# Kernel optimization log

Measured on AMD Instinct MI355X. Metric: run time of the kernel, lower is better.

## Reference

```python
import jax, jax.numpy as jnp
import numpy as np
from jax import lax

B, FREQ, TIME = 32, 256, 4096   # batch, freq bins, time frames
PAD_LEN = 256                   # cfg['n_peaks']
KSIZE = 5                       # cfg['blur_kernel']
SIGMA = 1.0                     # cfg['blur_sigma']


def setup_inputs() -> dict:
    key = jax.random.key(0)
    return {"spec_tensor": jax.random.normal(key, (B, FREQ, TIME), dtype=jnp.float32)}


def _peak_from_features(f):
    # local maxima along time (1x3) and freq (3x1), SAME padding, stride 1
    neg = jnp.asarray(-jnp.inf, f.dtype)
    max_t = lax.reduce_window(f, neg, lax.max, (1, 1, 3), (1, 1, 1), 'SAME')
    max_f = lax.reduce_window(f, neg, lax.max, (1, 3, 1), (1, 1, 1), 'SAME')
    peaks = ((f == max_t) & (f == max_f)).astype(f.dtype)
    mn = jnp.min(f, axis=(1, 2), keepdims=True)
    mx = jnp.max(f, axis=(1, 2), keepdims=True)
    return peaks * ((f - mn) / (mx - mn))


def _gaussian_blur(x):
    # separable gaussian blur with reflect padding (torchvision semantics)
    half = KSIZE // 2
    coords = jnp.arange(KSIZE, dtype=x.dtype) - half
    g = jnp.exp(-0.5 * (coords / SIGMA) ** 2)
    g = g / jnp.sum(g)
    x4 = jnp.pad(x, ((0, 0), (half, half), (half, half)), mode='reflect')[:, None]  # [B,1,F+2h,T+2h]
    kf = g.reshape(1, 1, KSIZE, 1)
    kt = g.reshape(1, 1, 1, KSIZE)
    y = lax.conv_general_dilated(x4, kf, (1, 1), 'VALID')
    y = lax.conv_general_dilated(y, kt, (1, 1), 'VALID')
    return y[:, 0]


def _extract(flat):
    # compact nonzero entries (row-major order) into fixed PAD_LEN slots, zero padded;
    # entries beyond PAD_LEN are truncated (scatter mode='drop').
    mask = flat > 0
    pos = jnp.cumsum(mask.astype(jnp.int32)) - 1
    dest = jnp.where(mask, pos, PAD_LEN)  # out-of-range -> dropped
    idx = jnp.zeros(PAD_LEN, jnp.int32).at[dest].set(
        jnp.arange(flat.shape[0], dtype=jnp.int32), mode='drop')
    val = jnp.zeros(PAD_LEN, flat.dtype).at[dest].set(flat, mode='drop')
    freq = (idx // TIME).astype(flat.dtype) / FREQ
    time = (idx % TIME).astype(flat.dtype) / TIME
    return jnp.stack([freq, time, val], axis=0)  # [3, PAD_LEN]


def reference(spec_tensor):
    p = _peak_from_features(spec_tensor)
    p = _gaussian_blur(p)
    p = _peak_from_features(p)
    return jax.vmap(_extract)(p.reshape(B, FREQ * TIME))  # [B, 3, PAD_LEN]
```

## Files before the change

kernel.cpp:

```cpp
#include <hip/hip_runtime.h>

#define NB 32
#define NF 256
#define NT 4096
#define PAD_LEN 256

#define TF 16
#define TT 128

#define TS 32
#define NSTRIP (NT / TS)

#define G0 0.054488684f
#define G1 0.24420134f
#define G2 0.40261995f

__device__ __forceinline__ float blur5(float a, float b, float c, float d, float e) {
    return G0 * (a + b) + G1 * (c + d) + G2 * e;
}
__device__ __forceinline__ float4 blur5v(const float4& a, const float4& b, const float4& c,
                                         const float4& d, const float4& e) {
    return make_float4(blur5(a.x, b.x, c.x, d.x, e.x), blur5(a.y, b.y, c.y, d.y, e.y),
                       blur5(a.z, b.z, c.z, d.z, e.z), blur5(a.w, b.w, c.w, d.w, e.w));
}

#define SW 140
#define SW4 35
#define RS 24
#define RP 22
#define RV 18

#define R1_WORDS (RS * SW)
#define R2_WORDS (RP * SW)

#define MPAD 12

__device__ __forceinline__ int reflectF(int i) {
    i = (i < 0) ? -i : i;
    return (i >= NF) ? (2 * NF - 2 - i) : i;
}
__device__ __forceinline__ unsigned encf(float x) {
    unsigned u = __float_as_uint(x);
    return (u & 0x80000000u) ? ~u : (u | 0x80000000u);
}
__device__ __forceinline__ float decf(unsigned e) {
    unsigned u = (e & 0x80000000u) ? (e ^ 0x80000000u) : ~e;
    return __uint_as_float(u);
}

#define MM_OFF 0
#define CNT_OFF 1024
#define PFX_OFF (1024 + NB * NF * 32 * 4)

__global__ __launch_bounds__(256) void k_init(float* __restrict__ out, unsigned* __restrict__ mm,
                                              int* __restrict__ counts2) {
    int tid = blockIdx.x * 256 + threadIdx.x;
    if (tid < NB * 3 * PAD_LEN) out[tid] = 0.0f;
    if (tid < NB) {
        mm[tid * 4 + 0] = 0xFFFFFFFFu;
        mm[tid * 4 + 1] = 0u;
        mm[tid * 4 + 2] = 0xFFFFFFFFu;
        mm[tid * 4 + 3] = 0u;
    }
    for (int i = tid; i < NB * NF * 32; i += 96 * 256) counts2[i] = 0;
}

__global__ __launch_bounds__(256) void k_minmax(const float* __restrict__ spec, unsigned* __restrict__ mm) {
    const int b = blockIdx.y;
    const float4* p = (const float4*)(spec + (size_t)b * NF * NT);
    const int base4 = blockIdx.x * 4096;
    float lmin = __builtin_inff(), lmax = -__builtin_inff();
    for (int i = threadIdx.x; i < 4096; i += 256) {
        float4 v = p[base4 + i];
        lmin = fminf(lmin, fminf(fminf(v.x, v.y), fminf(v.z, v.w)));
        lmax = fmaxf(lmax, fmaxf(fmaxf(v.x, v.y), fmaxf(v.z, v.w)));
    }
    for (int off = 32; off; off >>= 1) {
        lmin = fminf(lmin, __shfl_down(lmin, off));
        lmax = fmaxf(lmax, __shfl_down(lmax, off));
    }
    __shared__ float rmn[4], rmx[4];
    int wave = threadIdx.x >> 6, lane = threadIdx.x & 63;
    if (lane == 0) { rmn[wave] = lmin; rmx[wave] = lmax; }
    __syncthreads();
    if (threadIdx.x == 0) {
        for (int w = 1; w < 4; w++) { lmin = fminf(lmin, rmn[w]); lmax = fmaxf(lmax, rmx[w]); }
        atomicMin(&mm[b * 4 + 0], encf(lmin));
        atomicMax(&mm[b * 4 + 1], encf(lmax));
    }
}


template<int J> __device__ __forceinline__ float getj(const float4& v) {
    if constexpr (J == 0) return v.x;
    else if constexpr (J == 1) return v.y;
    else if constexpr (J == 2) return v.z;
    else return v.w;
}

template<bool DP, bool DH, bool DQ, int J>
__device__ __forceinline__ void march_step(
    const float4& r0, const float4& r1, const float4& r2, const float4& r3,
    float4& Sa, float4& Sb, float4& Sc,
    float4& V0, float4& V1, float4& V2, float4& V3, float4& V4,
    float4& Bm, float4& Bc, float4& Bp,
    int& c0, int& c1, int& c2, int& c3,
    float& lmin, float& lmax,
    const int lane, const int sid, const float mn, const float rinv, const int hb)
{
    const float NEGF = -__builtin_inff();
    float4 X = make_float4(getj<J>(r0), getj<J>(r1), getj<J>(r2), getj<J>(r3));
    Sa = Sb; Sb = Sc; Sc = X;
    if constexpr (DP) {
        float up0 = __shfl_up(Sb.w, 1);
        float dn3 = __shfl_down(Sb.x, 1);
        if (lane == 0)  up0 = NEGF;
        if (lane == 63) dn3 = NEGF;
        float4 P;
        { const float x = Sb.x; const bool pk = (x >= Sa.x) && (x >= Sc.x) && (x >= up0)  && (x >= Sb.y); P.x = pk ? (x - mn) * rinv : 0.0f; }
        { const float x = Sb.y; const bool pk = (x >= Sa.y) && (x >= Sc.y) && (x >= Sb.x) && (x >= Sb.z); P.y = pk ? (x - mn) * rinv : 0.0f; }
        { const float x = Sb.z; const bool pk = (x >= Sa.z) && (x >= Sc.z) && (x >= Sb.y) && (x >= Sb.w); P.z = pk ? (x - mn) * rinv : 0.0f; }
        { const float x = Sb.w; const bool pk = (x >= Sa.w) && (x >= Sc.w) && (x >= Sb.z) && (x >= dn3); P.w = pk ? (x - mn) * rinv : 0.0f; }
        const float pzm = __shfl_up(P.z, 1);
        const float pwm = __shfl_up(P.w, 1);
        const float pxp = __shfl_down(P.x, 1);
        const float pyp = __shfl_down(P.y, 1);
        float4 Vn;
        Vn.x = blur5(pzm, P.z, pwm, P.y, P.x);
        Vn.y = blur5(pwm, P.w, P.x, P.z, P.y);
        Vn.z = blur5(P.x, pxp, P.y, P.w, P.z);
        Vn.w = blur5(P.y, pyp, P.z, pxp, P.w);
        if (lane == 0)  { Vn.x = blur5(P.z, P.z, P.y, P.y, P.x);
                          Vn.y = blur5(P.y, P.w, P.x, P.z, P.y); }
        if (lane == 63) { Vn.z = blur5(P.x, P.z, P.y, P.w, P.z);
                          Vn.w = blur5(P.y, P.y, P.z, P.z, P.w); }
        V0 = V1; V1 = V2; V2 = V3; V3 = V4; V4 = Vn;
    }
    if constexpr (DH) {
        const int h = hb + J;
        float4 Bn;
        if ((unsigned)h < (unsigned)NT) {
            Bn = blur5v(V0, V4, V1, V3, V2);
            if (sid == 0) {
                if (h == 0)      Bn = blur5v(V4, V4, V3, V3, V2);
                else if (h == 1) Bn = blur5v(V2, V4, V1, V3, V2);
            }
            if (sid == NSTRIP - 1) {
                if (h == NT - 2)      Bn = blur5v(V0, V2, V1, V3, V2);
                else if (h == NT - 1) Bn = blur5v(V0, V0, V1, V1, V2);
            }
        } else {
            Bn = make_float4(NEGF, NEGF, NEGF, NEGF);
        }
        Bm = Bc; Bc = Bp; Bp = Bn;
    }
    if constexpr (DQ) {
        float u0 = __shfl_up(Bc.w, 1);
        float d3 = __shfl_down(Bc.x, 1);
        if (lane == 0)  u0 = NEGF;
        if (lane == 63) d3 = NEGF;
        { const float x = Bc.x; const bool pk = (x >= Bm.x) && (x >= Bp.x) && (x >= u0)   && (x >= Bc.y); c0 += (pk && (x > 0.0f)) ? 1 : 0; }
        { const float x = Bc.y; const bool pk = (x >= Bm.y) && (x >= Bp.y) && (x >= Bc.x) && (x >= Bc.z); c1 += (pk && (x > 0.0f)) ? 1 : 0; }
        { const float x = Bc.z; const bool pk = (x >= Bm.z) && (x >= Bp.z) && (x >= Bc.y) && (x >= Bc.w); c2 += (pk && (x > 0.0f)) ? 1 : 0; }
        { const float x = Bc.w; const bool pk = (x >= Bm.w) && (x >= Bp.w) && (x >= Bc.z) && (x >= d3); c3 += (pk && (x > 0.0f)) ? 1 : 0; }
        lmin = fminf(lmin, fminf(fminf(Bc.x, Bc.y), fminf(Bc.z, Bc.w)));
        lmax = fmaxf(lmax, fmaxf(fmaxf(Bc.x, Bc.y), fmaxf(Bc.z, Bc.w)));
    }
}

__global__ __launch_bounds__(256) void k_march(const float* __restrict__ spec,
                                               unsigned* __restrict__ mm,
                                               int* __restrict__ counts2) {
    const int b = blockIdx.y;
    const int lane = threadIdx.x & 63;
    const int wv = threadIdx.x >> 6;
    const int sid = blockIdx.x * 4 + wv;
    const int T0 = sid * TS;

    const float mn = decf(mm[b * 4 + 0]);
    const float mx = decf(mm[b * 4 + 1]);
    const float rinv = 1.0f / (mx - mn);

    const float NEGF = -__builtin_inff();
    const float4 NEG4 = make_float4(NEGF, NEGF, NEGF, NEGF);

    __shared__ __align__(16) float sStage[4][256 * MPAD];
    float* myS = sStage[wv];

    const int srow = lane >> 1;
    const int shalf = lane & 1;
    const float* gsrc = spec + (size_t)b * NF * NT + (size_t)srow * NT + 4 * shalf;

    float4 R[8];
    float4 A[4];

#define GLOAD(G) do {                                                          \
    const int tg = T0 - 4 + 8 * (G);                                           \
    const bool ok = (unsigned)(tg + 4 * shalf) < (unsigned)NT;                 \
    _Pragma("unroll")                                                          \
    for (int i = 0; i < 8; ++i)                                                \
        R[i] = ok ? *(const float4*)(gsrc + (size_t)(32 * i) * NT + tg) : NEG4; \
} while (0)

#define SWRITE() do {                                                          \
    _Pragma("unroll")                                                          \
    for (int i = 0; i < 8; ++i)                                                \
        *(float4*)(myS + (32 * i + srow) * MPAD + 4 * shalf) = R[i];           \
} while (0)

#define SREAD(c) do {                                                          \
    _Pragma("unroll")                                                          \
    for (int j = 0; j < 4; ++j)                                                \
        A[j] = *(const float4*)(myS + (4 * lane + j) * MPAD + (c));            \
} while (0)

    float4 Sa = NEG4, Sb = NEG4, Sc = NEG4;
    float4 V0 = NEG4, V1 = NEG4, V2 = NEG4, V3 = NEG4, V4 = NEG4;
    float4 Bm = NEG4, Bc = NEG4, Bp = NEG4;
    int c0 = 0, c1 = 0, c2 = 0, c3 = 0;
    float lmin = __builtin_inff(), lmax = NEGF;

#define MARGS Sa, Sb, Sc, V0, V1, V2, V3, V4, Bm, Bc, Bp, c0, c1, c2, c3, lmin, lmax, lane, sid, mn, rinv

    GLOAD(0);
    SWRITE();
    GLOAD(1);
    SREAD(0);
    march_step<false, false, false, 0>(A[0], A[1], A[2], A[3], MARGS, 0);
    march_step<false, false, false, 1>(A[0], A[1], A[2], A[3], MARGS, 0);
    march_step<true,  false, false, 2>(A[0], A[1], A[2], A[3], MARGS, 0);
    march_step<true,  false, false, 3>(A[0], A[1], A[2], A[3], MARGS, 0);
    SREAD(4);
    {
        const int hb = T0 - 3;
        march_step<true, false, false, 0>(A[0], A[1], A[2], A[3], MARGS, hb);
        march_step<true, false, false, 1>(A[0], A[1], A[2], A[3], MARGS, hb);
        march_step<true, true,  false, 2>(A[0], A[1], A[2], A[3], MARGS, hb);
        march_step<true, true,  false, 3>(A[0], A[1], A[2], A[3], MARGS, hb);
    }

#define STEADY_GROUP(G) do {                                                   \
    SWRITE();                                                                  \
    if ((G) < 4) GLOAD((G) + 1);                                               \
    SREAD(0);                                                                  \
    {                                                                          \
        const int hb = T0 + 8 * (G) - 7;           \
        march_step<true, true, true, 0>(A[0], A[1], A[2], A[3], MARGS, hb);    \
        march_step<true, true, true, 1>(A[0], A[1], A[2], A[3], MARGS, hb);    \
        march_step<true, true, true, 2>(A[0], A[1], A[2], A[3], MARGS, hb);    \
        march_step<true, true, true, 3>(A[0], A[1], A[2], A[3], MARGS, hb);    \
    }                                                                          \
    SREAD(4);                                                                  \
    {                                                                          \
        const int hb = T0 + 8 * (G) - 3;                         \
        march_step<true, true, true, 0>(A[0], A[1], A[2], A[3], MARGS, hb);    \
        march_step<true, true, true, 1>(A[0], A[1], A[2], A[3], MARGS, hb);    \
        march_step<true, true, true, 2>(A[0], A[1], A[2], A[3], MARGS, hb);    \
        march_step<true, true, true, 3>(A[0], A[1], A[2], A[3], MARGS, hb);    \
    }                                                                          \
} while (0)

    STEADY_GROUP(1);
    STEADY_GROUP(2);
    STEADY_GROUP(3);
    STEADY_GROUP(4);

#undef STEADY_GROUP
#undef GLOAD
#undef SWRITE
#undef SREAD
#undef MARGS

    const int fr = 4 * lane;
    const int cc = sid >> 2;
    atomicAdd(&counts2[(b * NF + fr + 0) * 32 + cc], c0);
    atomicAdd(&counts2[(b * NF + fr + 1) * 32 + cc], c1);
    atomicAdd(&counts2[(b * NF + fr + 2) * 32 + cc], c2);
    atomicAdd(&counts2[(b * NF + fr + 3) * 32 + cc], c3);

    for (int off = 32; off; off >>= 1) {
        lmin = fminf(lmin, __shfl_down(lmin, off));
        lmax = fmaxf(lmax, __shfl_down(lmax, off));
    }
    if (lane == 0) {
        atomicMin(&mm[b * 4 + 2], encf(lmin));
        atomicMax(&mm[b * 4 + 3], encf(lmax));
    }
}

__device__ __forceinline__ void blur_tile(const float* __restrict__ sb_base,
                                          int f0, int t0, float mn, float rinv,
                                          float* sR1, float* sR2, int tid,
                                          bool f_lo, bool f_hi, bool t_lo, bool t_hi) {
    const float NEG = -__builtin_inff();
    float* sS = sR1;
    float* sV = sR1;
    float* sB = sR2;
    float4* sS4 = (float4*)sR1;
    float4* sP4 = (float4*)sR2;
    float4* sV4 = (float4*)sR1;
    float4* sB4 = (float4*)sR2;

    const bool f_edge = f_lo || f_hi;
    const bool t_edge = t_lo || t_hi;
    const int lane = tid & 63;

    if (!f_edge && !t_edge) {
        const float4* gp = (const float4*)(sb_base + (size_t)(f0 - 4) * NT + (t0 - 4));
        for (int i = tid; i < RS * 34; i += 256) {
            int r = i / 34, c = i - r * 34;
            sS4[r * SW4 + c] = gp[r * (NT / 4) + c];
        }
    } else {
        for (int i = tid; i < RS * 34; i += 256) {
            int r = i / 34, c = i - r * 34;
            int gf = f0 - 4 + r;
            int gc0 = t0 - 4 + 4 * c;
            float4 v = make_float4(NEG, NEG, NEG, NEG);
            if ((unsigned)gf < NF && (unsigned)gc0 < NT)
                v = *(const float4*)(sb_base + (size_t)gf * NT + gc0);
            sS4[r * SW4 + c] = v;
        }
    }
    __syncthreads();

    for (int i = tid; i < RP * 34; i += 256) {
        int r = i / 34, g = i - r * 34;
        const float4 c4 = sS4[(r + 1) * SW4 + g];
        const float4 u4 = sS4[r * SW4 + g];
        const float4 d4 = sS4[(r + 2) * SW4 + g];
        float lm = __shfl_up(c4.w, 1);
        float rp = __shfl_down(c4.x, 1);
        if (lane == 0 && g > 0)   lm = sS[(r + 1) * SW + 4 * g - 1];
        if (lane == 63 && g < 33) rp = sS[(r + 1) * SW + 4 * g + 4];
        float4 o;
        o.x = (c4.x >= lm   && c4.x >= c4.y && c4.x >= u4.x && c4.x >= d4.x) ? (c4.x - mn) * rinv : 0.0f;
        o.y = (c4.y >= c4.x && c4.y >= c4.z && c4.y >= u4.y && c4.y >= d4.y) ? (c4.y - mn) * rinv : 0.0f;
        o.z = (c4.z >= c4.y && c4.z >= c4.w && c4.z >= u4.z && c4.z >= d4.z) ? (c4.z - mn) * rinv : 0.0f;
        o.w = (c4.w >= c4.z && c4.w >= rp   && c4.w >= u4.w && c4.w >= d4.w) ? (c4.w - mn) * rinv : 0.0f;
        if (g == 0) o.x = 0.0f;
        if (g == 33) o.w = 0.0f;
        sP4[r * SW4 + g] = o;
    }
    __syncthreads();

    if (!f_edge) {
        for (int i = tid; i < RV * 34; i += 256) {
            int r = i / 34, g = i - r * 34;
            const float4 p0 = sP4[r * SW4 + g];
            const float4 p1 = sP4[(r + 1) * SW4 + g];
            const float4 p2 = sP4[(r + 2) * SW4 + g];
            const float4 p3 = sP4[(r + 3) * SW4 + g];
            const float4 p4 = sP4[(r + 4) * SW4 + g];
            sV4[r * SW4 + g] = blur5v(p0, p4, p1, p3, p2);
        }
    } else {
        for (int i = tid; i < RV * 34; i += 256) {
            int r = i / 34, g = i - r * 34;
            const int gf = f0 - 1 + r;
            const int r0 = reflectF(gf - 2) - (f0 - 3);
            const int r1 = reflectF(gf - 1) - (f0 - 3);
            const int r2 = gf - (f0 - 3);
            const int r3 = reflectF(gf + 1) - (f0 - 3);
            const int r4 = reflectF(gf + 2) - (f0 - 3);
            const float4 p0 = sP4[r0 * SW4 + g];
            const float4 p1 = sP4[r1 * SW4 + g];
            const float4 p2 = sP4[r2 * SW4 + g];
            const float4 p3 = sP4[r3 * SW4 + g];
            const float4 p4 = sP4[r4 * SW4 + g];
            sV4[r * SW4 + g] = blur5v(p0, p4, p1, p3, p2);
        }
    }
    __syncthreads();

    for (int i = tid; i < RV * 32; i += 256) {
        int r = i >> 5, g = 1 + (i & 31);
        const float4 A = sV4[r * SW4 + g - 1];
        const float4 B = sV4[r * SW4 + g];
        const float4 C = sV4[r * SW4 + g + 1];
        float4 o;
        o.x = blur5(A.z, B.z, A.w, B.y, B.x);
        o.y = blur5(A.w, B.w, B.x, B.z, B.y);
        o.z = blur5(B.x, C.x, B.y, B.w, B.z);
        o.w = blur5(B.y, C.y, B.z, C.x, B.w);
        if (t_lo && g == 1) {
            o.x = blur5(B.z, B.z, B.y, B.y, B.x);
            o.y = blur5(B.y, B.w, B.x, B.z, B.y);
        }
        if (t_hi && g == 32) {
            o.z = blur5(B.x, B.z, B.y, B.w, B.z);
            o.w = blur5(B.y, B.y, B.z, B.z, B.w);
        }
        if ((f_lo && r == 0) || (f_hi && r == 17)) o = make_float4(NEG, NEG, NEG, NEG);
        sB4[r * SW4 + g] = o;
    }
    for (int i = tid; i < RV * 2; i += 256) {
        int r = i >> 1;
        int hi = i & 1;
        int s = hi ? 132 : 3;
        const float* vr = sV + r * SW;
        float v = blur5(vr[s - 2], vr[s + 2], vr[s - 1], vr[s + 1], vr[s]);
        if ((hi ? t_hi : t_lo) || (f_lo && r == 0) || (f_hi && r == 17)) v = NEG;
        sB[r * SW + s] = v;
    }
    __syncthreads();
}

struct Win8 {
    float c[8], l[8], rr[8], u[8], d[8];
};
__device__ __forceinline__ void load_win8(const float4* sB4, int r, int m, Win8& w) {
    const int g = 1 + 2 * m;
    const float4 Cm = sB4[(r + 1) * SW4 + g - 1];
    const float4 C0 = sB4[(r + 1) * SW4 + g];
    const float4 C1 = sB4[(r + 1) * SW4 + g + 1];
    const float4 C2 = sB4[(r + 1) * SW4 + g + 2];
    const float4 U0 = sB4[r * SW4 + g];
    const float4 U1 = sB4[r * SW4 + g + 1];
    const float4 D0 = sB4[(r + 2) * SW4 + g];
    const float4 D1 = sB4[(r + 2) * SW4 + g + 1];
    w.c[0] = C0.x; w.c[1] = C0.y; w.c[2] = C0.z; w.c[3] = C0.w;
    w.c[4] = C1.x; w.c[5] = C1.y; w.c[6] = C1.z; w.c[7] = C1.w;
    w.l[0] = Cm.w; w.l[1] = C0.x; w.l[2] = C0.y; w.l[3] = C0.z;
    w.l[4] = C0.w; w.l[5] = C1.x; w.l[6] = C1.y; w.l[7] = C1.z;
    w.rr[0] = C0.y; w.rr[1] = C0.z; w.rr[2] = C0.w; w.rr[3] = C1.x;
    w.rr[4] = C1.y; w.rr[5] = C1.z; w.rr[6] = C1.w; w.rr[7] = C2.x;
    w.u[0] = U0.x; w.u[1] = U0.y; w.u[2] = U0.z; w.u[3] = U0.w;
    w.u[4] = U1.x; w.u[5] = U1.y; w.u[6] = U1.z; w.u[7] = U1.w;
    w.d[0] = D0.x; w.d[1] = D0.y; w.d[2] = D0.z; w.d[3] = D0.w;
    w.d[4] = D1.x; w.d[5] = D1.y; w.d[6] = D1.z; w.d[7] = D1.w;
}

__global__ __launch_bounds__(256) void k_fallback(const float* __restrict__ spec, unsigned* __restrict__ mm,
                                                  int* __restrict__ counts2) {
    const int b = blockIdx.z;
    const float mn2 = decf(mm[b * 4 + 2]);
    if (mn2 == 0.0f) return;

    const int f0 = blockIdx.y * TF;
    const int t0 = blockIdx.x * TT;
    const int c0 = blockIdx.x;
    const int tid = threadIdx.x;

    __shared__ __align__(16) float sR1[R1_WORDS];
    __shared__ __align__(16) float sR2[R2_WORDS];
    const float4* sB4 = (const float4*)sR2;

    const float mn = decf(mm[b * 4 + 0]);
    const float mx = decf(mm[b * 4 + 1]);
    const float rinv = 1.0f / (mx - mn);
    const float* sb_base = spec + (size_t)b * NF * NT;

    const bool f_lo = (blockIdx.y == 0), f_hi = (blockIdx.y == NF / TF - 1);
    const bool t_lo = (blockIdx.x == 0), t_hi = (blockIdx.x == NT / TT - 1);
    blur_tile(sb_base, f0, t0, mn, rinv, sR1, sR2, tid, f_lo, f_hi, t_lo, t_hi);

    const int r = tid & 15, m = tid >> 4;
    Win8 w;
    load_win8(sB4, r, m, w);
    int cnt = 0;
#pragma unroll
    for (int k = 0; k < 8; k++) {
        float x = w.c[k];
        bool pk = (x >= w.l[k]) && (x >= w.rr[k]) && (x >= w.u[k]) && (x >= w.d[k]);
        cnt += (pk && (x > mn2)) ? 1 : 0;
    }
    __shared__ int pcnt[4][16];
    const int lane = tid & 63, wv = tid >> 6;
    int cs = cnt;
    cs += __shfl_down(cs, 32);
    cs += __shfl_down(cs, 16);
    if (lane < 16) pcnt[wv][lane] = cs;
    __syncthreads();
    if (tid < 16) {
        int tot = pcnt[0][tid] + pcnt[1][tid] + pcnt[2][tid] + pcnt[3][tid];
        counts2[(b * NF + f0 + tid) * 32 + c0] = tot;
    }
}

__global__ __launch_bounds__(256) void k_prefix(const int* __restrict__ counts2, int* __restrict__ prefix2) {
    const int b = blockIdx.x;
    const int tid = threadIdx.x;
    const int* cb = counts2 + b * NF * 32;
    int* pb = prefix2 + b * NF * 32;
    int local[32];
    int s = 0;
    for (int c = 0; c < 32; c++) {
        local[c] = cb[tid * 32 + c];
        s += local[c];
    }
    __shared__ int tot[256];
    tot[tid] = s;
    __syncthreads();
    for (int off = 1; off < 256; off <<= 1) {
        int v = (tid >= off) ? tot[tid - off] : 0;
        __syncthreads();
        tot[tid] += v;
        __syncthreads();
    }
    int run = tot[tid] - s;
    for (int c = 0; c < 32; c++) {
        pb[tid * 32 + c] = run;
        run += local[c];
    }
}

__global__ __launch_bounds__(256) void k_extract(const float* __restrict__ spec, unsigned* __restrict__ mm,
                                                 const int* __restrict__ prefix2, float* __restrict__ out) {
    const int b = blockIdx.z;
    const int f0 = blockIdx.y * TF;
    const int t0 = blockIdx.x * TT;
    const int c0 = blockIdx.x;
    if (prefix2[(b * NF + f0) * 32 + c0] >= PAD_LEN) return;

    const int tid = threadIdx.x;
    __shared__ __align__(16) float sR1[R1_WORDS];
    __shared__ __align__(16) float sR2[R2_WORDS];
    const float4* sB4 = (const float4*)sR2;

    const float mn = decf(mm[b * 4 + 0]);
    const float mx = decf(mm[b * 4 + 1]);
    const float rinv = 1.0f / (mx - mn);
    const float mn2 = decf(mm[b * 4 + 2]);
    const float mx2 = decf(mm[b * 4 + 3]);
    const float rinv2 = 1.0f / (mx2 - mn2);
    const float* sb_base = spec + (size_t)b * NF * NT;

    const bool f_lo = (blockIdx.y == 0), f_hi = (blockIdx.y == NF / TF - 1);
    const bool t_lo = (blockIdx.x == 0), t_hi = (blockIdx.x == NT / TT - 1);
    blur_tile(sb_base, f0, t0, mn, rinv, sR1, sR2, tid, f_lo, f_hi, t_lo, t_hi);

    const int r = tid & 15, m = tid >> 4;
    const int gf = f0 + r;
    const int base = prefix2[(b * NF + gf) * 32 + c0];
    Win8 w;
    load_win8(sB4, r, m, w);
    bool pos[8];
    int mycnt = 0;
#pragma unroll
    for (int k = 0; k < 8; k++) {
        float x = w.c[k];
        pos[k] = (x >= w.l[k]) && (x >= w.rr[k]) && (x >= w.u[k]) && (x >= w.d[k]) && (x > mn2);
        mycnt += pos[k] ? 1 : 0;
    }
    const int lane = tid & 63, wv = tid >> 6, p = (tid >> 4) & 3;
    int s = mycnt;
    int t1 = __shfl_up(s, 16); if (p >= 1) s += t1;
    int t2 = __shfl_up(s, 32); if (p >= 2) s += t2;
    __shared__ int wtot[4][16];
    if (p == 3) wtot[wv][lane & 15] = s;
    __syncthreads();
    int woff = 0;
    for (int w2 = 0; w2 < wv; ++w2) woff += wtot[w2][r];
    int rank = base + woff + (s - mycnt);
#pragma unroll
    for (int k = 0; k < 8; k++) {
        if (pos[k]) {
            if (rank < PAD_LEN) {
                int gc = t0 + 8 * m + k;
                out[b * 768 + rank]       = (float)gf * (1.0f / 256.0f);
                out[b * 768 + 256 + rank] = (float)gc * (1.0f / 4096.0f);
                out[b * 768 + 512 + rank] = (w.c[k] - mn2) * rinv2;
            }
            rank++;
        }
    }
}

extern "C" void kernel_launch(void* const* d_in, const int* in_sizes, int n_in,
                              void* d_out, int out_size, void* d_ws, size_t ws_size,
                              hipStream_t stream) {
    const float* spec = (const float*)d_in[0];
    float* out = (float*)d_out;
    unsigned* mm = (unsigned*)((char*)d_ws + MM_OFF);
    int* counts2 = (int*)((char*)d_ws + CNT_OFF);
    int* prefix2 = (int*)((char*)d_ws + PFX_OFF);

    k_init<<<96, 256, 0, stream>>>(out, mm, counts2);
    k_minmax<<<dim3(64, NB), 256, 0, stream>>>(spec, mm);
    k_march<<<dim3(NSTRIP / 4, NB), 256, 0, stream>>>(spec, mm, counts2);
    dim3 tgrid(NT / TT, NF / TF, NB);
    k_fallback<<<tgrid, 256, 0, stream>>>(spec, mm, counts2);
    k_prefix<<<NB, 256, 0, stream>>>(counts2, prefix2);
    k_extract<<<tgrid, 256, 0, stream>>>(spec, mm, prefix2, out);
}
```

Before: 382.0 us.

## Widen march strips, swizzle LDS staging, and fold fallback into prefix kernel

```diff
diff --git a/kernel.cpp b/kernel.cpp
--- a/kernel.cpp
+++ b/kernel.cpp
@@ -8,7 +8,7 @@
 #define TF 16
 #define TT 128
 
-#define TS 32
+#define TS 64
 #define NSTRIP (NT / TS)
 
 #define G0 0.054488684f
@@ -33,7 +33,7 @@
 #define R1_WORDS (RS * SW)
 #define R2_WORDS (RP * SW)
 
-#define MPAD 12
+#define MPAD 20
 
 __device__ __forceinline__ int reflectF(int i) {
     i = (i < 0) ? -i : i;
@@ -52,8 +52,7 @@
 #define CNT_OFF 1024
 #define PFX_OFF (1024 + NB * NF * 32 * 4)
 
-__global__ __launch_bounds__(256) void k_init(float* __restrict__ out, unsigned* __restrict__ mm,
-                                              int* __restrict__ counts2) {
+__global__ __launch_bounds__(256) void k_init(float* __restrict__ out, unsigned* __restrict__ mm) {
     int tid = blockIdx.x * 256 + threadIdx.x;
     if (tid < NB * 3 * PAD_LEN) out[tid] = 0.0f;
     if (tid < NB) {
@@ -62,7 +61,6 @@
         mm[tid * 4 + 2] = 0xFFFFFFFFu;
         mm[tid * 4 + 3] = 0u;
     }
-    for (int i = tid; i < NB * NF * 32; i += 96 * 256) counts2[i] = 0;
 }
 
 __global__ __launch_bounds__(256) void k_minmax(const float* __restrict__ spec, unsigned* __restrict__ mm) {
@@ -187,31 +185,42 @@
     __shared__ __align__(16) float sStage[4][256 * MPAD];
     float* myS = sStage[wv];
 
-    const int srow = lane >> 1;
-    const int shalf = lane & 1;
-    const float* gsrc = spec + (size_t)b * NF * NT + (size_t)srow * NT + 4 * shalf;
-
-    float4 R[8];
+    const int lrow = lane >> 2;
+    const int lq = lane & 3;
+    const float* gb = spec + (size_t)b * NF * NT;
+
+    float4 R[16];
     float4 A[4];
 
-#define GLOAD(G) do {                                                          \
-    const int tg = T0 - 4 + 8 * (G);                                           \
-    const bool ok = (unsigned)(tg + 4 * shalf) < (unsigned)NT;                 \
-    _Pragma("unroll")                                                          \
-    for (int i = 0; i < 8; ++i)                                                \
-        R[i] = ok ? *(const float4*)(gsrc + (size_t)(32 * i) * NT + tg) : NEG4; \
+#define GLOAD(J) do {                                                           \
+    const int tg = T0 - 16 + 16 * (J);                                          \
+    if ((unsigned)tg < (unsigned)NT) {                                          \
+        const float* gp = gb + (size_t)lrow * NT + tg + 4 * lq;                 \
+        _Pragma("unroll")                                                       \
+        for (int i = 0; i < 16; ++i)                                            \
+            R[i] = *(const float4*)(gp + (size_t)(16 * i) * NT);                \
+    } else {                                                                    \
+        _Pragma("unroll")                                                       \
+        for (int i = 0; i < 16; ++i) R[i] = NEG4;                               \
+    }                                                                           \
 } while (0)
 
-#define SWRITE() do {                                                          \
-    _Pragma("unroll")                                                          \
-    for (int i = 0; i < 8; ++i)                                                \
-        *(float4*)(myS + (32 * i + srow) * MPAD + 4 * shalf) = R[i];           \
+#define SWRITE() do {                                                           \
+    _Pragma("unroll")                                                           \
+    for (int i = 0; i < 16; ++i) {                                              \
+        const int row_ = 16 * i + lrow;                                         \
+        const int q_ = (row_ * 5 + lq) ^ ((row_ >> 2) & 7);                     \
+        *(float4*)(myS + 4 * q_) = R[i];                                        \
+    }                                                                           \
 } while (0)
 
-#define SREAD(c) do {                                                          \
-    _Pragma("unroll")                                                          \
-    for (int j = 0; j < 4; ++j)                                                \
-        A[j] = *(const float4*)(myS + (4 * lane + j) * MPAD + (c));            \
+#define SREAD(C) do {                                                           \
+    _Pragma("unroll")                                                           \
+    for (int j = 0; j < 4; ++j) {                                               \
+        const int row_ = 4 * lane + j;                                          \
+        const int q_ = (row_ * 5 + ((C) >> 2)) ^ (lane & 7);                    \
+        A[j] = *(const float4*)(myS + 4 * q_);                                  \
+    }                                                                           \
 } while (0)
 
     float4 Sa = NEG4, Sb = NEG4, Sc = NEG4;
@@ -222,61 +231,64 @@
 
 #define MARGS Sa, Sb, Sc, V0, V1, V2, V3, V4, Bm, Bc, Bp, c0, c1, c2, c3, lmin, lmax, lane, sid, mn, rinv
 
+#define SET_FULL(C, HB) do { SREAD(C); const int hb_ = (HB);                    \
+    march_step<true, true, true, 0>(A[0], A[1], A[2], A[3], MARGS, hb_);        \
+    march_step<true, true, true, 1>(A[0], A[1], A[2], A[3], MARGS, hb_);        \
+    march_step<true, true, true, 2>(A[0], A[1], A[2], A[3], MARGS, hb_);        \
+    march_step<true, true, true, 3>(A[0], A[1], A[2], A[3], MARGS, hb_); } while (0)
+
     GLOAD(0);
     SWRITE();
     GLOAD(1);
-    SREAD(0);
+    SREAD(12);
     march_step<false, false, false, 0>(A[0], A[1], A[2], A[3], MARGS, 0);
     march_step<false, false, false, 1>(A[0], A[1], A[2], A[3], MARGS, 0);
     march_step<true,  false, false, 2>(A[0], A[1], A[2], A[3], MARGS, 0);
     march_step<true,  false, false, 3>(A[0], A[1], A[2], A[3], MARGS, 0);
-    SREAD(4);
+    SWRITE();
+    GLOAD(2);
     {
-        const int hb = T0 - 3;
-        march_step<true, false, false, 0>(A[0], A[1], A[2], A[3], MARGS, hb);
-        march_step<true, false, false, 1>(A[0], A[1], A[2], A[3], MARGS, hb);
-        march_step<true, true,  false, 2>(A[0], A[1], A[2], A[3], MARGS, hb);
-        march_step<true, true,  false, 3>(A[0], A[1], A[2], A[3], MARGS, hb);
-    }
-
-#define STEADY_GROUP(G) do {                                                   \
-    SWRITE();                                                                  \
-    if ((G) < 4) GLOAD((G) + 1);                                               \
-    SREAD(0);                                                                  \
-    {                                                                          \
-        const int hb = T0 + 8 * (G) - 7;           \
-        march_step<true, true, true, 0>(A[0], A[1], A[2], A[3], MARGS, hb);    \
-        march_step<true, true, true, 1>(A[0], A[1], A[2], A[3], MARGS, hb);    \
-        march_step<true, true, true, 2>(A[0], A[1], A[2], A[3], MARGS, hb);    \
-        march_step<true, true, true, 3>(A[0], A[1], A[2], A[3], MARGS, hb);    \
-    }                                                                          \
-    SREAD(4);                                                                  \
-    {                                                                          \
-        const int hb = T0 + 8 * (G) - 3;                         \
-        march_step<true, true, true, 0>(A[0], A[1], A[2], A[3], MARGS, hb);    \
-        march_step<true, true, true, 1>(A[0], A[1], A[2], A[3], MARGS, hb);    \
-        march_step<true, true, true, 2>(A[0], A[1], A[2], A[3], MARGS, hb);    \
-        march_step<true, true, true, 3>(A[0], A[1], A[2], A[3], MARGS, hb);    \
-    }                                                                          \
-} while (0)
-
-    STEADY_GROUP(1);
-    STEADY_GROUP(2);
-    STEADY_GROUP(3);
-    STEADY_GROUP(4);
-
-#undef STEADY_GROUP
+        const int hb_ = T0 - 3;
+        SREAD(0);
+        march_step<true, false, false, 0>(A[0], A[1], A[2], A[3], MARGS, hb_);
+        march_step<true, false, false, 1>(A[0], A[1], A[2], A[3], MARGS, hb_);
+        march_step<true, true,  false, 2>(A[0], A[1], A[2], A[3], MARGS, hb_);
+        march_step<true, true,  false, 3>(A[0], A[1], A[2], A[3], MARGS, hb_);
+    }
+    SET_FULL(4,  T0 + 1);
+    SET_FULL(8,  T0 + 5);
+    SET_FULL(12, T0 + 9);
+    SWRITE(); GLOAD(3);
+    SET_FULL(0,  T0 + 13); SET_FULL(4,  T0 + 17); SET_FULL(8,  T0 + 21); SET_FULL(12, T0 + 25);
+    SWRITE(); GLOAD(4);
+    SET_FULL(0,  T0 + 29); SET_FULL(4,  T0 + 33); SET_FULL(8,  T0 + 37); SET_FULL(12, T0 + 41);
+    SWRITE(); GLOAD(5);
+    SET_FULL(0,  T0 + 45); SET_FULL(4,  T0 + 49); SET_FULL(8,  T0 + 53); SET_FULL(12, T0 + 57);
+    SWRITE();
+    SET_FULL(0,  T0 + 61);
+
+#undef SET_FULL
 #undef GLOAD
 #undef SWRITE
 #undef SREAD
 #undef MARGS
 
-    const int fr = 4 * lane;
-    const int cc = sid >> 2;
-    atomicAdd(&counts2[(b * NF + fr + 0) * 32 + cc], c0);
-    atomicAdd(&counts2[(b * NF + fr + 1) * 32 + cc], c1);
-    atomicAdd(&counts2[(b * NF + fr + 2) * 32 + cc], c2);
-    atomicAdd(&counts2[(b * NF + fr + 3) * 32 + cc], c3);
+    int* sc = (int*)&sStage[0][0];
+    __syncthreads();
+    sc[threadIdx.x * 4 + 0] = c0;
+    sc[threadIdx.x * 4 + 1] = c1;
+    sc[threadIdx.x * 4 + 2] = c2;
+    sc[threadIdx.x * 4 + 3] = c3;
+    __syncthreads();
+    if ((wv & 1) == 0) {
+        const int p = (threadIdx.x + 64) * 4;
+        const int cc = sid >> 1;
+        const int fr = 4 * lane;
+        counts2[(b * NF + fr + 0) * 32 + cc] = c0 + sc[p + 0];
+        counts2[(b * NF + fr + 1) * 32 + cc] = c1 + sc[p + 1];
+        counts2[(b * NF + fr + 2) * 32 + cc] = c2 + sc[p + 2];
+        counts2[(b * NF + fr + 3) * 32 + cc] = c3 + sc[p + 3];
+    }
 
     for (int off = 32; off; off >>= 1) {
         lmin = fminf(lmin, __shfl_down(lmin, off));
@@ -431,56 +443,49 @@
     w.d[4] = D1.x; w.d[5] = D1.y; w.d[6] = D1.z; w.d[7] = D1.w;
 }
 
-__global__ __launch_bounds__(256) void k_fallback(const float* __restrict__ spec, unsigned* __restrict__ mm,
-                                                  int* __restrict__ counts2) {
-    const int b = blockIdx.z;
-    const float mn2 = decf(mm[b * 4 + 2]);
-    if (mn2 == 0.0f) return;
-
-    const int f0 = blockIdx.y * TF;
-    const int t0 = blockIdx.x * TT;
-    const int c0 = blockIdx.x;
-    const int tid = threadIdx.x;
-
-    __shared__ __align__(16) float sR1[R1_WORDS];
-    __shared__ __align__(16) float sR2[R2_WORDS];
-    const float4* sB4 = (const float4*)sR2;
-
-    const float mn = decf(mm[b * 4 + 0]);
-    const float mx = decf(mm[b * 4 + 1]);
-    const float rinv = 1.0f / (mx - mn);
-    const float* sb_base = spec + (size_t)b * NF * NT;
-
-    const bool f_lo = (blockIdx.y == 0), f_hi = (blockIdx.y == NF / TF - 1);
-    const bool t_lo = (blockIdx.x == 0), t_hi = (blockIdx.x == NT / TT - 1);
-    blur_tile(sb_base, f0, t0, mn, rinv, sR1, sR2, tid, f_lo, f_hi, t_lo, t_hi);
-
-    const int r = tid & 15, m = tid >> 4;
-    Win8 w;
-    load_win8(sB4, r, m, w);
-    int cnt = 0;
-#pragma unroll
-    for (int k = 0; k < 8; k++) {
-        float x = w.c[k];
-        bool pk = (x >= w.l[k]) && (x >= w.rr[k]) && (x >= w.u[k]) && (x >= w.d[k]);
-        cnt += (pk && (x > mn2)) ? 1 : 0;
-    }
-    __shared__ int pcnt[4][16];
-    const int lane = tid & 63, wv = tid >> 6;
-    int cs = cnt;
-    cs += __shfl_down(cs, 32);
-    cs += __shfl_down(cs, 16);
-    if (lane < 16) pcnt[wv][lane] = cs;
-    __syncthreads();
-    if (tid < 16) {
-        int tot = pcnt[0][tid] + pcnt[1][tid] + pcnt[2][tid] + pcnt[3][tid];
-        counts2[(b * NF + f0 + tid) * 32 + c0] = tot;
-    }
-}
-
-__global__ __launch_bounds__(256) void k_prefix(const int* __restrict__ counts2, int* __restrict__ prefix2) {
+__global__ __launch_bounds__(256) void k_prefix(const float* __restrict__ spec,
+                                                unsigned* __restrict__ mm,
+                                                int* __restrict__ counts2,
+                                                int* __restrict__ prefix2) {
     const int b = blockIdx.x;
     const int tid = threadIdx.x;
+    const float mn2 = decf(mm[b * 4 + 2]);
+    if (mn2 != 0.0f) {
+        __shared__ __align__(16) float sR1[R1_WORDS];
+        __shared__ __align__(16) float sR2[R2_WORDS];
+        const float4* sB4 = (const float4*)sR2;
+        const float mn = decf(mm[b * 4 + 0]);
+        const float mx = decf(mm[b * 4 + 1]);
+        const float rinv = 1.0f / (mx - mn);
+        const float* sb_base = spec + (size_t)b * NF * NT;
+        int* pcnt = (int*)sR1;
+        for (int ty = 0; ty < NF / TF; ++ty)
+        for (int tx = 0; tx < NT / TT; ++tx) {
+            blur_tile(sb_base, ty * TF, tx * TT, mn, rinv, sR1, sR2, tid,
+                      ty == 0, ty == NF / TF - 1, tx == 0, tx == NT / TT - 1);
+            const int r = tid & 15, m = tid >> 4;
+            Win8 w;
+            load_win8(sB4, r, m, w);
+            int cnt = 0;
+#pragma unroll
+            for (int k = 0; k < 8; k++) {
+                float x = w.c[k];
+                bool pk = (x >= w.l[k]) && (x >= w.rr[k]) && (x >= w.u[k]) && (x >= w.d[k]);
+                cnt += (pk && (x > mn2)) ? 1 : 0;
+            }
+            (void)m;
+            const int lane = tid & 63, wvv = tid >> 6;
+            int cs = cnt;
+            cs += __shfl_down(cs, 32);
+            cs += __shfl_down(cs, 16);
+            if (lane < 16) pcnt[wvv * 16 + lane] = cs;
+            __syncthreads();
+            if (tid < 16)
+                counts2[(b * NF + ty * TF + tid) * 32 + tx] =
+                    pcnt[tid] + pcnt[16 + tid] + pcnt[32 + tid] + pcnt[48 + tid];
+            __syncthreads();
+        }
+    }
     const int* cb = counts2 + b * NF * 32;
     int* pb = prefix2 + b * NF * 32;
     int local[32];
@@ -576,11 +581,10 @@
     int* counts2 = (int*)((char*)d_ws + CNT_OFF);
     int* prefix2 = (int*)((char*)d_ws + PFX_OFF);
 
-    k_init<<<96, 256, 0, stream>>>(out, mm, counts2);
+    k_init<<<96, 256, 0, stream>>>(out, mm);
     k_minmax<<<dim3(64, NB), 256, 0, stream>>>(spec, mm);
     k_march<<<dim3(NSTRIP / 4, NB), 256, 0, stream>>>(spec, mm, counts2);
+    k_prefix<<<NB, 256, 0, stream>>>(spec, mm, counts2, prefix2);
     dim3 tgrid(NT / TT, NF / TF, NB);
-    k_fallback<<<tgrid, 256, 0, stream>>>(spec, mm, counts2);
-    k_prefix<<<NB, 256, 0, stream>>>(counts2, prefix2);
     k_extract<<<tgrid, 256, 0, stream>>>(spec, mm, prefix2, out);
 }
```

Result: faster. 330.7 us (-13.4%).
